# Kernel optimization log

Measured on AMD Instinct MI355X. Metric: run time of the kernel, lower is better.

The kernel has to match this reference:

```python
import jax, jax.numpy as jnp
import numpy as np

OUT_H, OUT_W = 7, 7
SPATIAL_SCALE = 0.0625
N_IMG, C, H, W = 2, 256, 38, 38
NUM_ROIS = 256
IMG_MAX = 607.9  # keeps floor(coord*scale) <= 37


def setup_inputs() -> dict:
    key = jax.random.key(0)
    k_feat, k_b, k_xa, k_xb, k_ya, k_yb = jax.random.split(key, 6)
    feat = jax.random.normal(k_feat, (N_IMG, C, H, W), dtype=jnp.float32)
    bidx = jax.random.randint(k_b, (NUM_ROIS,), 0, N_IMG).astype(jnp.float32)
    xa = jax.random.uniform(k_xa, (NUM_ROIS,), minval=0.0, maxval=IMG_MAX)
    xb = jax.random.uniform(k_xb, (NUM_ROIS,), minval=0.0, maxval=IMG_MAX)
    ya = jax.random.uniform(k_ya, (NUM_ROIS,), minval=0.0, maxval=IMG_MAX)
    yb = jax.random.uniform(k_yb, (NUM_ROIS,), minval=0.0, maxval=IMG_MAX)
    rois = jnp.stack([bidx,
                      jnp.minimum(xa, xb), jnp.minimum(ya, yb),
                      jnp.maximum(xa, xb), jnp.maximum(ya, yb)], axis=1)
    return {"input": feat, "rois": rois.astype(jnp.float32)}


def _roi_max_pool(feat_all, rois):
    # feat_all: (N, C, H, W); rois: (R, 5) = (batch_idx, x1, y1, x2, y2)
    H_, W_ = feat_all.shape[2], feat_all.shape[3]
    b = rois[:, 0].astype(jnp.int32)
    # torch: rois[:,1:].mul_(scale); rois.long() -> truncation (== floor for >=0)
    coords = jnp.floor(rois[:, 1:] * SPATIAL_SCALE).astype(jnp.int32)
    x1, y1, x2, y2 = coords[:, 0], coords[:, 1], coords[:, 2], coords[:, 3]
    rh = y2 - y1 + 1  # inclusive crop: [y1, y2+1)
    rw = x2 - x1 + 1
    feat = feat_all[b]  # (R, C, H, W) per-ROI gather of its image
    neg = jnp.array(-jnp.inf, feat.dtype)

    # separable adaptive max pool: rows then cols
    hs = jnp.arange(H_)
    rows = []
    for i in range(OUT_H):  # fixed small loop over output bins
        hstart = y1 + (i * rh) // OUT_H                       # floor(i*rh/OUT_H)
        hend = y1 + ((i + 1) * rh + OUT_H - 1) // OUT_H       # ceil
        m = (hs[None, :] >= hstart[:, None]) & (hs[None, :] < hend[:, None])  # (R,H)
        rows.append(jnp.max(jnp.where(m[:, None, :, None], feat, neg), axis=2))  # (R,C,W)
    rowmax = jnp.stack(rows, axis=2)  # (R, C, OUT_H, W)

    ws = jnp.arange(W_)
    cols = []
    for j in range(OUT_W):
        wstart = x1 + (j * rw) // OUT_W
        wend = x1 + ((j + 1) * rw + OUT_W - 1) // OUT_W
        m = (ws[None, :] >= wstart[:, None]) & (ws[None, :] < wend[:, None])  # (R,W)
        cols.append(jnp.max(jnp.where(m[:, None, None, :], rowmax, neg), axis=3))  # (R,C,OUT_H)
    return jnp.stack(cols, axis=3)  # (R, C, OUT_H, OUT_W)


def reference(input, rois):
    return _roi_max_pool(input, rois)
```

## Files before the change

### kernel.cpp

```cpp
#include <hip/hip_runtime.h>
#include <math.h>

#define OUT_H 7
#define OUT_W 7
#define N_C 256
#define FH 38
#define FW 38
#define NUM_ROIS 256
#define SPATIAL_SCALE 0.0625f

__global__ __launch_bounds__(256) void roi_pool_kernel(
    const float* __restrict__ feat,
    const float* __restrict__ rois,
    float* __restrict__ out)
{
    int t = blockIdx.x * blockDim.x + threadIdx.x;

    int j = t % OUT_W;
    int i = (t / OUT_W) % OUT_H;
    int c = (t / (OUT_W * OUT_H)) % N_C;
    int r = t / (OUT_W * OUT_H * N_C);

    const float* roi = rois + r * 5;
    int b  = (int)roi[0];
    int x1 = (int)(roi[1] * SPATIAL_SCALE);
    int y1 = (int)(roi[2] * SPATIAL_SCALE);
    int x2 = (int)(roi[3] * SPATIAL_SCALE);
    int y2 = (int)(roi[4] * SPATIAL_SCALE);
    int rh = y2 - y1 + 1;
    int rw = x2 - x1 + 1;

    int hstart = y1 + (i * rh) / OUT_H;
    int hend   = y1 + ((i + 1) * rh + OUT_H - 1) / OUT_H;
    int wstart = x1 + (j * rw) / OUT_W;
    int wend   = x1 + ((j + 1) * rw + OUT_W - 1) / OUT_W;

    const float* fp = feat + ((size_t)b * N_C + c) * (FH * FW);
    float m = -INFINITY;
    for (int h = hstart; h < hend; ++h) {
        const float* row = fp + h * FW;
        for (int w = wstart; w < wend; ++w) {
            m = fmaxf(m, row[w]);
        }
    }
    out[t] = m;
}

extern "C" void kernel_launch(void* const* d_in, const int* in_sizes, int n_in,
                              void* d_out, int out_size, void* d_ws, size_t ws_size,
                              hipStream_t stream) {
    const float* feat = (const float*)d_in[0];
    const float* rois = (const float*)d_in[1];
    float* out = (float*)d_out;

    int total = NUM_ROIS * N_C * OUT_H * OUT_W;
    int block = 256;
    int grid = (total + block - 1) / block;
    roi_pool_kernel<<<grid, block, 0, stream>>>(feat, rois, out);
}
```

Measured before the change: 79.97 us.

## Use separable row-then-column max pooling with shared-memory staging per ROI channel chunk

Each block now handles one ROI and a chunk of 8 channels. It first computes per-row-bin column maxima over the full feature width and stores them in shared memory, then reduces across columns to produce the output bins. This removes redundant reads that overlapping bins caused in the naive per-output-element loop, and the row pass reads contiguous w so global loads coalesce. The cost is a shared-memory round trip and a barrier, plus row-pass work over all 38 columns even when the ROI is narrow.

```diff
diff --git a/kernel.cpp b/kernel.cpp
--- a/kernel.cpp
+++ b/kernel.cpp
@@ -9,41 +9,63 @@
 #define NUM_ROIS 256
 #define SPATIAL_SCALE 0.0625f
 
+#define CC 8
+#define CHUNKS (N_C / CC)
+
 __global__ __launch_bounds__(256) void roi_pool_kernel(
     const float* __restrict__ feat,
     const float* __restrict__ rois,
     float* __restrict__ out)
 {
-    int t = blockIdx.x * blockDim.x + threadIdx.x;
+    __shared__ float rowmax[CC][OUT_H][FW];
 
-    int j = t % OUT_W;
-    int i = (t / OUT_W) % OUT_H;
-    int c = (t / (OUT_W * OUT_H)) % N_C;
-    int r = t / (OUT_W * OUT_H * N_C);
+    int blk   = blockIdx.x;
+    int r     = blk / CHUNKS;
+    int chunk = blk - r * CHUNKS;
+    int c0    = chunk * CC;
 
     const float* roi = rois + r * 5;
-    int b  = (int)roi[0];
-    int x1 = (int)(roi[1] * SPATIAL_SCALE);
-    int y1 = (int)(roi[2] * SPATIAL_SCALE);
-    int x2 = (int)(roi[3] * SPATIAL_SCALE);
-    int y2 = (int)(roi[4] * SPATIAL_SCALE);
+    int b  = __builtin_amdgcn_readfirstlane((int)roi[0]);
+    int x1 = __builtin_amdgcn_readfirstlane((int)(roi[1] * SPATIAL_SCALE));
+    int y1 = __builtin_amdgcn_readfirstlane((int)(roi[2] * SPATIAL_SCALE));
+    int x2 = __builtin_amdgcn_readfirstlane((int)(roi[3] * SPATIAL_SCALE));
+    int y2 = __builtin_amdgcn_readfirstlane((int)(roi[4] * SPATIAL_SCALE));
     int rh = y2 - y1 + 1;
     int rw = x2 - x1 + 1;
 
-    int hstart = y1 + (i * rh) / OUT_H;
-    int hend   = y1 + ((i + 1) * rh + OUT_H - 1) / OUT_H;
-    int wstart = x1 + (j * rw) / OUT_W;
-    int wend   = x1 + ((j + 1) * rw + OUT_W - 1) / OUT_W;
+    int tid = threadIdx.x;
 
-    const float* fp = feat + ((size_t)b * N_C + c) * (FH * FW);
-    float m = -INFINITY;
-    for (int h = hstart; h < hend; ++h) {
-        const float* row = fp + h * FW;
-        for (int w = wstart; w < wend; ++w) {
-            m = fmaxf(m, row[w]);
-        }
+    const int TA = CC * OUT_H * FW;
+    const float* fbase = feat + ((size_t)b * N_C + c0) * (FH * FW);
+    for (int task = tid; task < TA; task += 256) {
+        int w  = task % FW;
+        int iw = task / FW;
+        int i  = iw % OUT_H;
+        int cl = iw / OUT_H;
+        int hstart = y1 + (i * rh) / OUT_H;
+        int hend   = y1 + ((i + 1) * rh + OUT_H - 1) / OUT_H;
+        const float* fp = fbase + cl * (FH * FW) + w;
+        float m = -INFINITY;
+        for (int h = hstart; h < hend; ++h)
+            m = fmaxf(m, fp[h * FW]);
+        rowmax[cl][i][w] = m;
     }
-    out[t] = m;
+    __syncthreads();
+
+    const int TB = CC * OUT_H * OUT_W;
+    float* obase = out + ((size_t)r * N_C + c0) * (OUT_H * OUT_W);
+    for (int task = tid; task < TB; task += 256) {
+        int pos = task % (OUT_H * OUT_W);
+        int cl  = task / (OUT_H * OUT_W);
+        int i   = pos / OUT_W;
+        int j   = pos - i * OUT_W;
+        int wstart = x1 + (j * rw) / OUT_W;
+        int wend   = x1 + ((j + 1) * rw + OUT_W - 1) / OUT_W;
+        float m = -INFINITY;
+        for (int w = wstart; w < wend; ++w)
+            m = fmaxf(m, rowmax[cl][i][w]);
+        obase[task] = m;
+    }
 }
 
 extern "C" void kernel_launch(void* const* d_in, const int* in_sizes, int n_in,
@@ -53,8 +75,7 @@
     const float* rois = (const float*)d_in[1];
     float* out = (float*)d_out;
 
-    int total = NUM_ROIS * N_C * OUT_H * OUT_W;
+    int grid  = NUM_ROIS * CHUNKS;
     int block = 256;
-    int grid = (total + block - 1) / block;
     roi_pool_kernel<<<grid, block, 0, stream>>>(feat, rois, out);
 }
```

Result: slower. 97.33 us (+21.7%).
